# Kernel optimization log

Hardware: AMD Instinct MI355X
Metric: run time of the kernel (lower is better)

## Reference

```python
import jax, jax.numpy as jnp
import numpy as np

B, NDOC, L, E = 32, 4, 512, 512
SCALE = np.float32(1.0 / np.sqrt(E))
NEG_INF = np.float32(-1e9)


def setup_inputs() -> dict:
    key = jax.random.key(0)
    k1, k2, k3, k4, k5, k6 = jax.random.split(key, 6)
    return {
        "x1": jax.random.normal(k1, (B, L, E), dtype=jnp.float32),
        "x2": jax.random.normal(k2, (B, NDOC, L, E), dtype=jnp.float32),
        "x1_len": jax.random.randint(k3, (B,), 0, L, dtype=jnp.int64),
        "x2_len": jax.random.randint(k4, (B, NDOC), 0, L, dtype=jnp.int64),
        "fusion_w": jax.random.normal(k5, (2 * E, E), dtype=jnp.float32) * 0.02,
        "fusion_b": jnp.zeros((E,), dtype=jnp.float32),
        "out_w": jax.random.normal(k6, (8 * E, 2 * E), dtype=jnp.float32) * 0.02,
        "out_b": jnp.zeros((2 * E,), dtype=jnp.float32),
    }


def reference(x1, x2, x1_len, x2_len, fusion_w, fusion_b, out_w, out_b):
    # Faithful to torch .repeat(1,4,...): concatenate 4 full copies along batch,
    # so attention row i pairs x1[i % B] with x2[i // 4, i % 4].
    x1_rep = jnp.tile(x1, (NDOC, 1, 1))          # [4B, L, E]
    x2_r = x2.reshape(-1, L, E)                  # [4B, L, E]

    x1_len_r = jnp.tile(x1_len, NDOC)            # [4B] (same tiling as x1_rep)
    x2_len_r = x2_len.reshape(-1)                # [4B]
    pos = jnp.arange(L)
    q_mask = pos[None, :] < x1_len_r[:, None]    # [4B, L]
    k_mask = pos[None, :] < x2_len_r[:, None]    # [4B, L]
    mask = q_mask[:, :, None] & k_mask[:, None, :]  # [4B, L, L]

    # scaled-dot-product attention with masked_fill(mask==0, -1e9)
    scores = jnp.einsum('bqe,bke->bqk', x1_rep, x2_r) * SCALE  # [4B, L, L]
    scores = jnp.where(mask, scores, NEG_INF)
    attn = jax.nn.softmax(scores, axis=-1)
    x1_att = jnp.einsum('bqk,bke->bqe', attn, x2_r)            # [4B, L, E]

    cat = jnp.concatenate([x1_rep - x1_att, x1_rep * x1_att], axis=-1)  # [4B, L, 2E]
    fus = jax.nn.relu(cat @ fusion_w + fusion_b)                        # [4B, L, E]

    x1_mean = jnp.mean(fus, axis=1)              # [4B, E]
    x1_max = jnp.max(fus, axis=1)                # [4B, E]
    pooled = jnp.concatenate([x1_mean.reshape(B, -1), x1_max.reshape(B, -1)], axis=-1)  # [B, 8E]
    out = jax.nn.relu(pooled @ out_w + out_b)    # [B, 2E]
    return out, attn
```

## Files before the change

### kernel.cpp

```cpp
#include <hip/hip_runtime.h>
#include <cstddef>

#define BATCH 32
#define NB    128
#define LL    512
#define EE    512
#define SCALE 0.044194173824159216f
#define NEG_INF -1e9f

typedef __attribute__((ext_vector_type(4))) float f32x4;
typedef __attribute__((ext_vector_type(8))) short s16x8;
typedef __attribute__((ext_vector_type(4))) unsigned short u16x4;

__device__ __forceinline__ unsigned short f2b(float f) {
    unsigned u = __float_as_uint(f);
    u += 0x7FFFu + ((u >> 16) & 1u);
    return (unsigned short)(u >> 16);
}
__device__ __forceinline__ float b2f(unsigned short h) {
    return __uint_as_float(((unsigned)h) << 16);
}

__device__ __forceinline__ void gld_lds16(const unsigned short* g, unsigned short* l) {
    __builtin_amdgcn_global_load_lds(
        (const __attribute__((address_space(1))) void*)g,
        (__attribute__((address_space(3))) void*)l, 16, 0, 0);
}

__global__ __launch_bounds__(256) void k_cvt_x1(
    const float* __restrict__ x1, unsigned short* __restrict__ x1bf)
{
    const size_t idx = (size_t)blockIdx.x * 256 + threadIdx.x;
    f32x4 v = *(const f32x4*)(x1 + idx * 4);
    u16x4 o = { f2b(v[0]), f2b(v[1]), f2b(v[2]), f2b(v[3]) };
    *(u16x4*)(x1bf + idx * 4) = o;
}

__global__ __launch_bounds__(256) void k_cvt_x2(
    const float* __restrict__ x2,
    unsigned short* __restrict__ x2bf, unsigned short* __restrict__ x2t)
{
    __shared__ float T[64][65];
    const int i = blockIdx.z, kb = blockIdx.y * 64, eb = blockIdx.x * 64;
    const float* src = x2 + (size_t)i * LL * EE;
    unsigned short* db = x2bf + (size_t)i * LL * EE;
    unsigned short* dt = x2t  + (size_t)i * LL * EE;
    const int t = threadIdx.x, r16 = t >> 4, c4 = (t & 15) * 4;
#pragma unroll
    for (int p = 0; p < 4; ++p) {
        int row = p * 16 + r16;
        f32x4 v = *(const f32x4*)(src + (size_t)(kb + row) * EE + eb + c4);
        T[row][c4] = v[0]; T[row][c4+1] = v[1]; T[row][c4+2] = v[2]; T[row][c4+3] = v[3];
        u16x4 o = { f2b(v[0]), f2b(v[1]), f2b(v[2]), f2b(v[3]) };
        *(u16x4*)(db + (size_t)(kb + row) * EE + eb + c4) = o;
    }
    __syncthreads();
#pragma unroll
    for (int p = 0; p < 4; ++p) {
        int erow = p * 16 + r16;
        u16x4 o = { f2b(T[c4][erow]), f2b(T[c4+1][erow]),
                    f2b(T[c4+2][erow]), f2b(T[c4+3][erow]) };
        *(u16x4*)(dt + (size_t)(eb + erow) * LL + kb + c4) = o;
    }
}

__global__ __launch_bounds__(256) void k_cvt_fw(
    const float* __restrict__ fw, unsigned short* __restrict__ fwt)
{
    __shared__ float T[64][65];
    const int jb = blockIdx.y * 64, eb = blockIdx.x * 64;
    const int t = threadIdx.x, r16 = t >> 4, c4 = (t & 15) * 4;
#pragma unroll
    for (int p = 0; p < 4; ++p) {
        int row = p * 16 + r16;
        f32x4 v = *(const f32x4*)(fw + (size_t)(jb + row) * EE + eb + c4);
        T[row][c4] = v[0]; T[row][c4+1] = v[1]; T[row][c4+2] = v[2]; T[row][c4+3] = v[3];
    }
    __syncthreads();
#pragma unroll
    for (int p = 0; p < 4; ++p) {
        int erow = p * 16 + r16;
#pragma unroll
        for (int k = 0; k < 4; ++k) {
            int jold = jb + c4 + k;
            int jn = (jold < 512) ? (2 * jold) : (2 * (jold - 512) + 1);
            fwt[(size_t)(eb + erow) * 1024 + jn] = f2b(T[c4 + k][erow]);
        }
    }
}

__global__ __launch_bounds__(256) void k_scores_mfma(
    const unsigned short* __restrict__ x1bf,
    const unsigned short* __restrict__ x2bf,
    const int* __restrict__ x1_len, const int* __restrict__ x2_len,
    float* __restrict__ attn)
{
    __shared__ unsigned short Al[128 * 32];
    __shared__ unsigned short Bl[128 * 32];
    const int i  = blockIdx.x;
    const int q0 = (blockIdx.y >> 2) * 128;
    const int k0 = (blockIdx.y & 3) * 128;
    const unsigned short* Ag = x1bf + (size_t)(i & 31) * LL * EE;
    const unsigned short* Bg = x2bf + (size_t)i * LL * EE;
    const int t = threadIdx.x, lane = t & 63;
    const int w = t >> 6, wrow = w >> 1, wcol = w & 1;
    const int m = lane & 15, quad = lane >> 4;
    const int lrow = lane >> 2, lcol = (lane & 3) * 8;

    f32x4 acc[4][4];
#pragma unroll
    for (int r = 0; r < 4; ++r)
#pragma unroll
        for (int c = 0; c < 4; ++c) acc[r][c] = (f32x4){0.f, 0.f, 0.f, 0.f};

    for (int e0 = 0; e0 < EE; e0 += 32) {
#pragma unroll
        for (int c = 0; c < 2; ++c) {
            const int s = c * 4 + w;
            gld_lds16(Ag + (size_t)(q0 + s * 16 + lrow) * EE + e0 + lcol, &Al[s * 512]);
            gld_lds16(Bg + (size_t)(k0 + s * 16 + lrow) * EE + e0 + lcol, &Bl[s * 512]);
        }
        __syncthreads();
        s16x8 af[4], bfr[4];
#pragma unroll
        for (int rt = 0; rt < 4; ++rt)
            af[rt] = *(const s16x8*)&Al[(wrow * 64 + rt * 16 + m) * 32 + quad * 8];
#pragma unroll
        for (int ct = 0; ct < 4; ++ct)
            bfr[ct] = *(const s16x8*)&Bl[(wcol * 64 + ct * 16 + m) * 32 + quad * 8];
#pragma unroll
        for (int rt = 0; rt < 4; ++rt)
#pragma unroll
            for (int ct = 0; ct < 4; ++ct)
                acc[rt][ct] = __builtin_amdgcn_mfma_f32_16x16x32_bf16(
                    af[rt], bfr[ct], acc[rt][ct], 0, 0, 0);
        __syncthreads();
    }

    const int qlen = x1_len[i & 31];
    const int klen = x2_len[i];
    float* op = attn + (size_t)i * LL * LL;
#pragma unroll
    for (int rt = 0; rt < 4; ++rt) {
#pragma unroll
        for (int reg = 0; reg < 4; ++reg) {
            const int q = q0 + wrow * 64 + rt * 16 + quad * 4 + reg;
            const bool qok = q < qlen;
#pragma unroll
            for (int ct = 0; ct < 4; ++ct) {
                const int k = k0 + wcol * 64 + ct * 16 + m;
                float v = (qok && k < klen) ? acc[rt][ct][reg] * SCALE : NEG_INF;
                op[(size_t)q * LL + k] = v;
            }
        }
    }
}

__global__ __launch_bounds__(256) void k_softmax(
    float* __restrict__ attn, unsigned short* __restrict__ attnbf)
{
    const int row  = blockIdx.x * 4 + (threadIdx.x >> 6);
    const int lane = threadIdx.x & 63;
    float* p = attn + (size_t)row * LL + lane * 8;
    float4 v0 = *(float4*)p;
    float4 v1 = *(float4*)(p + 4);
    float mx = fmaxf(fmaxf(fmaxf(v0.x, v0.y), fmaxf(v0.z, v0.w)),
                     fmaxf(fmaxf(v1.x, v1.y), fmaxf(v1.z, v1.w)));
#pragma unroll
    for (int o = 32; o > 0; o >>= 1) mx = fmaxf(mx, __shfl_xor(mx, o));
    v0.x = __expf(v0.x - mx); v0.y = __expf(v0.y - mx);
    v0.z = __expf(v0.z - mx); v0.w = __expf(v0.w - mx);
    v1.x = __expf(v1.x - mx); v1.y = __expf(v1.y - mx);
    v1.z = __expf(v1.z - mx); v1.w = __expf(v1.w - mx);
    float s = v0.x + v0.y + v0.z + v0.w + v1.x + v1.y + v1.z + v1.w;
#pragma unroll
    for (int o = 32; o > 0; o >>= 1) s += __shfl_xor(s, o);
    const float inv = 1.0f / s;
    v0.x *= inv; v0.y *= inv; v0.z *= inv; v0.w *= inv;
    v1.x *= inv; v1.y *= inv; v1.z *= inv; v1.w *= inv;
    *(float4*)p = v0;
    *(float4*)(p + 4) = v1;
    unsigned short* pb = attnbf + (size_t)row * LL + lane * 8;
    u16x4 o0 = { f2b(v0.x), f2b(v0.y), f2b(v0.z), f2b(v0.w) };
    u16x4 o1 = { f2b(v1.x), f2b(v1.y), f2b(v1.z), f2b(v1.w) };
    *(u16x4*)pb       = o0;
    *(u16x4*)(pb + 4) = o1;
}

__global__ __launch_bounds__(256) void k_pv_mfma(
    const unsigned short* __restrict__ attnbf,
    const unsigned short* __restrict__ x2t,
    const unsigned short* __restrict__ x1bf,
    unsigned short* __restrict__ Cbuf)
{
    __shared__ unsigned short Al[128 * 32];
    __shared__ unsigned short Bl[128 * 32];
    const int i  = blockIdx.x;
    const int q0 = (blockIdx.y >> 2) * 128;
    const int e0 = (blockIdx.y & 3) * 128;
    const unsigned short* Ag = attnbf + (size_t)i * LL * LL;
    const unsigned short* Bg = x2t   + (size_t)i * LL * EE;
    const int t = threadIdx.x, lane = t & 63;
    const int w = t >> 6, wrow = w >> 1, wcol = w & 1;
    const int m = lane & 15, quad = lane >> 4;
    const int lrow = lane >> 2, lcol = (lane & 3) * 8;

    f32x4 acc[4][4];
#pragma unroll
    for (int r = 0; r < 4; ++r)
#pragma unroll
        for (int c = 0; c < 4; ++c) acc[r][c] = (f32x4){0.f, 0.f, 0.f, 0.f};

    for (int kk0 = 0; kk0 < LL; kk0 += 32) {
#pragma unroll
        for (int c = 0; c < 2; ++c) {
            const int s = c * 4 + w;
            gld_lds16(Ag + (size_t)(q0 + s * 16 + lrow) * LL + kk0 + lcol, &Al[s * 512]);
            gld_lds16(Bg + (size_t)(e0 + s * 16 + lrow) * LL + kk0 + lcol, &Bl[s * 512]);
        }
        __syncthreads();
        s16x8 af[4], bfr[4];
#pragma unroll
        for (int rt = 0; rt < 4; ++rt)
            af[rt] = *(const s16x8*)&Al[(wrow * 64 + rt * 16 + m) * 32 + quad * 8];
#pragma unroll
        for (int ct = 0; ct < 4; ++ct)
            bfr[ct] = *(const s16x8*)&Bl[(wcol * 64 + ct * 16 + m) * 32 + quad * 8];
#pragma unroll
        for (int rt = 0; rt < 4; ++rt)
#pragma unroll
            for (int ct = 0; ct < 4; ++ct)
                acc[rt][ct] = __builtin_amdgcn_mfma_f32_16x16x32_bf16(
                    af[rt], bfr[ct], acc[rt][ct], 0, 0, 0);
        __syncthreads();
    }

    const unsigned short* x1p = x1bf + (size_t)(i & 31) * LL * EE;
    unsigned short* Cb = Cbuf + (size_t)i * LL * 1024;
#pragma unroll
    for (int rt = 0; rt < 4; ++rt) {
#pragma unroll
        for (int reg = 0; reg < 4; ++reg) {
            const int l = q0 + wrow * 64 + rt * 16 + quad * 4 + reg;
#pragma unroll
            for (int ct = 0; ct < 4; ++ct) {
                const int e = e0 + wcol * 64 + ct * 16 + m;
                float att = acc[rt][ct][reg];
                float xv  = b2f(x1p[(size_t)l * EE + e]);
                unsigned pr = (unsigned)f2b(xv - att) | ((unsigned)f2b(xv * att) << 16);
                *(unsigned*)(Cb + (size_t)l * 1024 + 2 * e) = pr;
            }
        }
    }
}

__global__ __launch_bounds__(256) void k_fuse_mfma(
    const unsigned short* __restrict__ Cbuf,
    const unsigned short* __restrict__ fwt,
    const float* __restrict__ fb,
    float* __restrict__ pmean, float* __restrict__ pmax)
{
    __shared__ unsigned short Al[128 * 32];
    __shared__ unsigned short Bl[128 * 32];
    __shared__ float psum[2][128];
    __shared__ float pmx[2][128];
    const int i  = blockIdx.x;
    const int lt = blockIdx.y >> 2;
    const int e0 = (blockIdx.y & 3) * 128;
    const unsigned short* Ab = Cbuf + ((size_t)i * LL + lt * 128) * 1024;
    const int t = threadIdx.x, lane = t & 63;
    const int w = t >> 6, wrow = w >> 1, wcol = w & 1;
    const int m = lane & 15, quad = lane >> 4;
    const int lrow = lane >> 2, lcol = (lane & 3) * 8;

    float bias[4];
#pragma unroll
    for (int ct = 0; ct < 4; ++ct) bias[ct] = fb[e0 + wcol * 64 + ct * 16 + m];
    float csum[4] = {0.f, 0.f, 0.f, 0.f};
    float cmax[4] = {-3e38f, -3e38f, -3e38f, -3e38f};

    f32x4 acc[4][4];
#pragma unroll
    for (int r = 0; r < 4; ++r)
#pragma unroll
        for (int c = 0; c < 4; ++c) acc[r][c] = (f32x4){0.f, 0.f, 0.f, 0.f};

    for (int j0 = 0; j0 < 1024; j0 += 32) {
#pragma unroll
        for (int c = 0; c < 2; ++c) {
            const int s = c * 4 + w;
            gld_lds16(Ab + (size_t)(s * 16 + lrow) * 1024 + j0 + lcol, &Al[s * 512]);
            gld_lds16(fwt + (size_t)(e0 + s * 16 + lrow) * 1024 + j0 + lcol, &Bl[s * 512]);
        }
        __syncthreads();
        s16x8 af[4], bfr[4];
#pragma unroll
        for (int rt = 0; rt < 4; ++rt)
            af[rt] = *(const s16x8*)&Al[(wrow * 64 + rt * 16 + m) * 32 + quad * 8];
#pragma unroll
        for (int ct = 0; ct < 4; ++ct)
            bfr[ct] = *(const s16x8*)&Bl[(wcol * 64 + ct * 16 + m) * 32 + quad * 8];
#pragma unroll
        for (int rt = 0; rt < 4; ++rt)
#pragma unroll
            for (int ct = 0; ct < 4; ++ct)
                acc[rt][ct] = __builtin_amdgcn_mfma_f32_16x16x32_bf16(
                    af[rt], bfr[ct], acc[rt][ct], 0, 0, 0);
        __syncthreads();
    }
#pragma unroll
    for (int rt = 0; rt < 4; ++rt)
#pragma unroll
        for (int reg = 0; reg < 4; ++reg)
#pragma unroll
            for (int ct = 0; ct < 4; ++ct) {
                float f = fmaxf(acc[rt][ct][reg] + bias[ct], 0.f);
                csum[ct] += f;
                cmax[ct] = fmaxf(cmax[ct], f);
            }
#pragma unroll
    for (int ct = 0; ct < 4; ++ct) {
        csum[ct] += __shfl_xor(csum[ct], 16);
        csum[ct] += __shfl_xor(csum[ct], 32);
        cmax[ct] = fmaxf(cmax[ct], __shfl_xor(cmax[ct], 16));
        cmax[ct] = fmaxf(cmax[ct], __shfl_xor(cmax[ct], 32));
    }
    if (quad == 0) {
#pragma unroll
        for (int ct = 0; ct < 4; ++ct) {
            psum[wrow][wcol * 64 + ct * 16 + m] = csum[ct];
            pmx[wrow][wcol * 64 + ct * 16 + m] = cmax[ct];
        }
    }
    __syncthreads();
    if (t < 128) {
        float s  = psum[0][t] + psum[1][t];
        float mx = fmaxf(pmx[0][t], pmx[1][t]);
        pmean[((size_t)i * 4 + lt) * EE + e0 + t] = s;
        pmax[((size_t)i * 4 + lt) * EE + e0 + t]  = mx;
    }
}

__global__ __launch_bounds__(256) void k_out_split(
    const float* __restrict__ pmean, const float* __restrict__ pmax,
    const float* __restrict__ ow, float* __restrict__ partial)
{
    __shared__ float ps[256];
    const int kc = blockIdx.x;
    const int b  = blockIdx.y;
    const int t  = threadIdx.x;
    const int j  = kc * 256 + t;
    const int jj = (j < 2048) ? j : j - 2048;
    const int ii = 4 * b + (jj >> 9);
    const int e  = jj & 511;
    float v;
    if (j < 2048) {
        const float* bp = pmean + (size_t)ii * 4 * EE + e;
        v = (bp[0] + bp[512] + bp[1024] + bp[1536]) * (1.0f / 512.0f);
    } else {
        const float* bp = pmax + (size_t)ii * 4 * EE + e;
        v = fmaxf(fmaxf(bp[0], bp[512]), fmaxf(bp[1024], bp[1536]));
    }
    ps[t] = v;
    __syncthreads();
    f32x4 acc = {0.f, 0.f, 0.f, 0.f};
    const float* wp = ow + (size_t)kc * 256 * 1024 + t * 4;
#pragma unroll 8
    for (int q = 0; q < 256; ++q) {
        f32x4 w4 = *(const f32x4*)(wp + (size_t)q * 1024);
        float p = ps[q];
        acc[0] = fmaf(p, w4[0], acc[0]);
        acc[1] = fmaf(p, w4[1], acc[1]);
        acc[2] = fmaf(p, w4[2], acc[2]);
        acc[3] = fmaf(p, w4[3], acc[3]);
    }
    *(f32x4*)(partial + ((size_t)kc * 32 + b) * 1024 + t * 4) = acc;
}

__global__ __launch_bounds__(256) void k_out_final(
    const float* __restrict__ partial, const float* __restrict__ ob,
    float* __restrict__ out)
{
    const int idx = blockIdx.x * 256 + threadIdx.x;
    const int b = idx >> 10, o = idx & 1023;
    float s = ob[o];
#pragma unroll
    for (int kc = 0; kc < 16; ++kc)
        s += partial[((size_t)kc * 32 + b) * 1024 + o];
    out[idx] = fmaxf(s, 0.f);
}

extern "C" void kernel_launch(void* const* d_in, const int* in_sizes, int n_in,
                              void* d_out, int out_size, void* d_ws, size_t ws_size,
                              hipStream_t stream)
{
    const float* x1     = (const float*)d_in[0];
    const float* x2     = (const float*)d_in[1];
    const int*   x1_len = (const int*)d_in[2];
    const int*   x2_len = (const int*)d_in[3];
    const float* fw     = (const float*)d_in[4];
    const float* fb     = (const float*)d_in[5];
    const float* ow     = (const float*)d_in[6];
    const float* ob     = (const float*)d_in[7];

    float* out  = (float*)d_out;
    float* attn = out + (size_t)BATCH * 1024;

    char* wp = (char*)d_ws;
    unsigned short* x1bf   = (unsigned short*)wp; wp += (size_t)BATCH * LL * EE * 2;
    unsigned short* x2bf   = (unsigned short*)wp; wp += (size_t)NB * LL * EE * 2;
    unsigned short* x2t    = (unsigned short*)wp; wp += (size_t)NB * LL * EE * 2;
    unsigned short* attnbf = (unsigned short*)wp; wp += (size_t)NB * LL * LL * 2;
    unsigned short* Cbuf   = (unsigned short*)wp; wp += (size_t)NB * LL * 1024 * 2;
    unsigned short* fwt    = (unsigned short*)wp; wp += (size_t)EE * 1024 * 2;
    float* pmean   = (float*)wp; wp += (size_t)NB * 4 * EE * 4;
    float* pmax    = (float*)wp; wp += (size_t)NB * 4 * EE * 4;
    float* partial = (float*)wp; wp += (size_t)16 * BATCH * 1024 * 4;

    k_cvt_x1<<<dim3(BATCH * LL * EE / 4 / 256), 256, 0, stream>>>(x1, x1bf);
    k_cvt_x2<<<dim3(8, 8, NB), 256, 0, stream>>>(x2, x2bf, x2t);
    k_cvt_fw<<<dim3(8, 16), 256, 0, stream>>>(fw, fwt);
    k_scores_mfma<<<dim3(128, 16), 256, 0, stream>>>(x1bf, x2bf, x1_len, x2_len, attn);
    k_softmax<<<dim3(NB * LL / 4), 256, 0, stream>>>(attn, attnbf);
    k_pv_mfma<<<dim3(128, 16), 256, 0, stream>>>(attnbf, x2t, x1bf, Cbuf);
    k_fuse_mfma<<<dim3(128, 16), 256, 0, stream>>>(Cbuf, fwt, fb, pmean, pmax);
    k_out_split<<<dim3(16, BATCH), 256, 0, stream>>>(pmean, pmax, ow, partial);
    k_out_final<<<dim3(BATCH * 1024 / 256), 256, 0, stream>>>(partial, ob, out);
}
```

Baseline: 637.0 us.

## Fuse scores, softmax and PV into one full-row attention kernel

```diff
diff --git a/kernel.cpp b/kernel.cpp
--- a/kernel.cpp
+++ b/kernel.cpp
@@ -89,23 +89,30 @@
     }
 }
 
-__global__ __launch_bounds__(256) void k_scores_mfma(
+__global__ __launch_bounds__(1024, 4) void k_attn(
     const unsigned short* __restrict__ x1bf,
     const unsigned short* __restrict__ x2bf,
+    const unsigned short* __restrict__ x2t,
     const int* __restrict__ x1_len, const int* __restrict__ x2_len,
-    float* __restrict__ attn)
-{
-    __shared__ unsigned short Al[128 * 32];
-    __shared__ unsigned short Bl[128 * 32];
+    float* __restrict__ attn, unsigned short* __restrict__ Cbuf)
+{
+    __shared__ __align__(16) char smem[147456];
+    unsigned short* Ast = (unsigned short*)smem;
+    unsigned short* Bst = (unsigned short*)(smem + 8192);
+    unsigned short* Bpv = (unsigned short*)(smem + 131072);
+    float* rowred = (float*)(smem + 131072);
+    float* rowst  = (float*)(smem + 131072 + 4096);
+
     const int i  = blockIdx.x;
-    const int q0 = (blockIdx.y >> 2) * 128;
-    const int k0 = (blockIdx.y & 3) * 128;
+    const int q0 = blockIdx.y * 128;
     const unsigned short* Ag = x1bf + (size_t)(i & 31) * LL * EE;
     const unsigned short* Bg = x2bf + (size_t)i * LL * EE;
+    const unsigned short* Vg = x2t  + (size_t)i * LL * EE;
     const int t = threadIdx.x, lane = t & 63;
-    const int w = t >> 6, wrow = w >> 1, wcol = w & 1;
+    const int w = t >> 6;
     const int m = lane & 15, quad = lane >> 4;
     const int lrow = lane >> 2, lcol = (lane & 3) * 8;
+    const int wrow = w >> 3, wcol = w & 7;
 
     f32x4 acc[4][4];
 #pragma unroll
@@ -114,20 +121,18 @@
         for (int c = 0; c < 4; ++c) acc[r][c] = (f32x4){0.f, 0.f, 0.f, 0.f};
 
     for (int e0 = 0; e0 < EE; e0 += 32) {
-#pragma unroll
-        for (int c = 0; c < 2; ++c) {
-            const int s = c * 4 + w;
-            gld_lds16(Ag + (size_t)(q0 + s * 16 + lrow) * EE + e0 + lcol, &Al[s * 512]);
-            gld_lds16(Bg + (size_t)(k0 + s * 16 + lrow) * EE + e0 + lcol, &Bl[s * 512]);
-        }
+        if (w < 8)
+            gld_lds16(Ag + (size_t)(q0 + w * 16 + lrow) * EE + e0 + lcol, &Ast[w * 512]);
+        gld_lds16(Bg + (size_t)((2 * w) * 16 + lrow) * EE + e0 + lcol, &Bst[(2 * w) * 512]);
+        gld_lds16(Bg + (size_t)((2 * w + 1) * 16 + lrow) * EE + e0 + lcol, &Bst[(2 * w + 1) * 512]);
         __syncthreads();
         s16x8 af[4], bfr[4];
 #pragma unroll
         for (int rt = 0; rt < 4; ++rt)
-            af[rt] = *(const s16x8*)&Al[(wrow * 64 + rt * 16 + m) * 32 + quad * 8];
+            af[rt] = *(const s16x8*)&Ast[(wrow * 64 + rt * 16 + m) * 32 + quad * 8];
 #pragma unroll
         for (int ct = 0; ct < 4; ++ct)
-            bfr[ct] = *(const s16x8*)&Bl[(wcol * 64 + ct * 16 + m) * 32 + quad * 8];
+            bfr[ct] = *(const s16x8*)&Bst[(wcol * 64 + ct * 16 + m) * 32 + quad * 8];
 #pragma unroll
         for (int rt = 0; rt < 4; ++rt)
 #pragma unroll
@@ -139,118 +144,135 @@
 
     const int qlen = x1_len[i & 31];
     const int klen = x2_len[i];
-    float* op = attn + (size_t)i * LL * LL;
-#pragma unroll
-    for (int rt = 0; rt < 4; ++rt) {
-#pragma unroll
-        for (int reg = 0; reg < 4; ++reg) {
-            const int q = q0 + wrow * 64 + rt * 16 + quad * 4 + reg;
-            const bool qok = q < qlen;
-#pragma unroll
-            for (int ct = 0; ct < 4; ++ct) {
-                const int k = k0 + wcol * 64 + ct * 16 + m;
-                float v = (qok && k < klen) ? acc[rt][ct][reg] * SCALE : NEG_INF;
-                op[(size_t)q * LL + k] = v;
-            }
-        }
-    }
-}
-
-__global__ __launch_bounds__(256) void k_softmax(
-    float* __restrict__ attn, unsigned short* __restrict__ attnbf)
-{
-    const int row  = blockIdx.x * 4 + (threadIdx.x >> 6);
-    const int lane = threadIdx.x & 63;
-    float* p = attn + (size_t)row * LL + lane * 8;
-    float4 v0 = *(float4*)p;
-    float4 v1 = *(float4*)(p + 4);
-    float mx = fmaxf(fmaxf(fmaxf(v0.x, v0.y), fmaxf(v0.z, v0.w)),
-                     fmaxf(fmaxf(v1.x, v1.y), fmaxf(v1.z, v1.w)));
-#pragma unroll
-    for (int o = 32; o > 0; o >>= 1) mx = fmaxf(mx, __shfl_xor(mx, o));
-    v0.x = __expf(v0.x - mx); v0.y = __expf(v0.y - mx);
-    v0.z = __expf(v0.z - mx); v0.w = __expf(v0.w - mx);
-    v1.x = __expf(v1.x - mx); v1.y = __expf(v1.y - mx);
-    v1.z = __expf(v1.z - mx); v1.w = __expf(v1.w - mx);
-    float s = v0.x + v0.y + v0.z + v0.w + v1.x + v1.y + v1.z + v1.w;
-#pragma unroll
-    for (int o = 32; o > 0; o >>= 1) s += __shfl_xor(s, o);
-    const float inv = 1.0f / s;
-    v0.x *= inv; v0.y *= inv; v0.z *= inv; v0.w *= inv;
-    v1.x *= inv; v1.y *= inv; v1.z *= inv; v1.w *= inv;
-    *(float4*)p = v0;
-    *(float4*)(p + 4) = v1;
-    unsigned short* pb = attnbf + (size_t)row * LL + lane * 8;
-    u16x4 o0 = { f2b(v0.x), f2b(v0.y), f2b(v0.z), f2b(v0.w) };
-    u16x4 o1 = { f2b(v1.x), f2b(v1.y), f2b(v1.z), f2b(v1.w) };
-    *(u16x4*)pb       = o0;
-    *(u16x4*)(pb + 4) = o1;
-}
-
-__global__ __launch_bounds__(256) void k_pv_mfma(
-    const unsigned short* __restrict__ attnbf,
-    const unsigned short* __restrict__ x2t,
-    const unsigned short* __restrict__ x1bf,
-    unsigned short* __restrict__ Cbuf)
-{
-    __shared__ unsigned short Al[128 * 32];
-    __shared__ unsigned short Bl[128 * 32];
-    const int i  = blockIdx.x;
-    const int q0 = (blockIdx.y >> 2) * 128;
-    const int e0 = (blockIdx.y & 3) * 128;
-    const unsigned short* Ag = attnbf + (size_t)i * LL * LL;
-    const unsigned short* Bg = x2t   + (size_t)i * LL * EE;
-    const int t = threadIdx.x, lane = t & 63;
-    const int w = t >> 6, wrow = w >> 1, wcol = w & 1;
-    const int m = lane & 15, quad = lane >> 4;
-    const int lrow = lane >> 2, lcol = (lane & 3) * 8;
-
-    f32x4 acc[4][4];
-#pragma unroll
-    for (int r = 0; r < 4; ++r)
-#pragma unroll
-        for (int c = 0; c < 4; ++c) acc[r][c] = (f32x4){0.f, 0.f, 0.f, 0.f};
-
-    for (int kk0 = 0; kk0 < LL; kk0 += 32) {
-#pragma unroll
-        for (int c = 0; c < 2; ++c) {
-            const int s = c * 4 + w;
-            gld_lds16(Ag + (size_t)(q0 + s * 16 + lrow) * LL + kk0 + lcol, &Al[s * 512]);
-            gld_lds16(Bg + (size_t)(e0 + s * 16 + lrow) * LL + kk0 + lcol, &Bl[s * 512]);
-        }
-        __syncthreads();
-        s16x8 af[4], bfr[4];
-#pragma unroll
-        for (int rt = 0; rt < 4; ++rt)
-            af[rt] = *(const s16x8*)&Al[(wrow * 64 + rt * 16 + m) * 32 + quad * 8];
-#pragma unroll
-        for (int ct = 0; ct < 4; ++ct)
-            bfr[ct] = *(const s16x8*)&Bl[(wcol * 64 + ct * 16 + m) * 32 + quad * 8];
-#pragma unroll
-        for (int rt = 0; rt < 4; ++rt)
-#pragma unroll
-            for (int ct = 0; ct < 4; ++ct)
-                acc[rt][ct] = __builtin_amdgcn_mfma_f32_16x16x32_bf16(
-                    af[rt], bfr[ct], acc[rt][ct], 0, 0, 0);
-        __syncthreads();
-    }
-
-    const unsigned short* x1p = x1bf + (size_t)(i & 31) * LL * EE;
-    unsigned short* Cb = Cbuf + (size_t)i * LL * 1024;
-#pragma unroll
-    for (int rt = 0; rt < 4; ++rt) {
+
+#pragma unroll
+    for (int rt = 0; rt < 4; ++rt)
 #pragma unroll
         for (int reg = 0; reg < 4; ++reg) {
             const int l = q0 + wrow * 64 + rt * 16 + quad * 4 + reg;
+            const bool qok = l < qlen;
 #pragma unroll
             for (int ct = 0; ct < 4; ++ct) {
-                const int e = e0 + wcol * 64 + ct * 16 + m;
-                float att = acc[rt][ct][reg];
-                float xv  = b2f(x1p[(size_t)l * EE + e]);
-                unsigned pr = (unsigned)f2b(xv - att) | ((unsigned)f2b(xv * att) << 16);
-                *(unsigned*)(Cb + (size_t)l * 1024 + 2 * e) = pr;
-            }
-        }
+                const int k = wcol * 64 + ct * 16 + m;
+                acc[rt][ct][reg] = (qok && k < klen) ? acc[rt][ct][reg] * SCALE : NEG_INF;
+            }
+        }
+
+#pragma unroll
+    for (int rt = 0; rt < 4; ++rt)
+#pragma unroll
+        for (int reg = 0; reg < 4; ++reg) {
+            float v = fmaxf(fmaxf(acc[rt][0][reg], acc[rt][1][reg]),
+                            fmaxf(acc[rt][2][reg], acc[rt][3][reg]));
+            v = fmaxf(v, __shfl_xor(v, 1));
+            v = fmaxf(v, __shfl_xor(v, 2));
+            v = fmaxf(v, __shfl_xor(v, 4));
+            v = fmaxf(v, __shfl_xor(v, 8));
+            if (m == 0)
+                rowred[wcol * 128 + wrow * 64 + rt * 16 + quad * 4 + reg] = v;
+        }
+    __syncthreads();
+    if (t < 128) {
+        float mx = rowred[t];
+#pragma unroll
+        for (int c = 1; c < 8; ++c) mx = fmaxf(mx, rowred[c * 128 + t]);
+        rowst[t] = mx;
+    }
+    __syncthreads();
+
+#pragma unroll
+    for (int rt = 0; rt < 4; ++rt)
+#pragma unroll
+        for (int reg = 0; reg < 4; ++reg) {
+            const int lloc = wrow * 64 + rt * 16 + quad * 4 + reg;
+            const float mx = rowst[lloc];
+            float s = 0.f;
+#pragma unroll
+            for (int ct = 0; ct < 4; ++ct) {
+                float p = __expf(acc[rt][ct][reg] - mx);
+                acc[rt][ct][reg] = p;
+                s += p;
+            }
+            s += __shfl_xor(s, 1);
+            s += __shfl_xor(s, 2);
+            s += __shfl_xor(s, 4);
+            s += __shfl_xor(s, 8);
+            if (m == 0) rowred[wcol * 128 + lloc] = s;
+        }
+    __syncthreads();
+    if (t < 128) {
+        float s = 0.f;
+#pragma unroll
+        for (int c = 0; c < 8; ++c) s += rowred[c * 128 + t];
+        rowst[t] = 1.0f / s;
+    }
+    __syncthreads();
+
+    float* op = attn + (size_t)i * LL * LL;
+#pragma unroll
+    for (int rt = 0; rt < 4; ++rt)
+#pragma unroll
+        for (int reg = 0; reg < 4; ++reg) {
+            const int lloc = wrow * 64 + rt * 16 + quad * 4 + reg;
+            const float inv = rowst[lloc];
+#pragma unroll
+            for (int ct = 0; ct < 4; ++ct) {
+                const int k = wcol * 64 + ct * 16 + m;
+                float p = acc[rt][ct][reg] * inv;
+                op[(size_t)(q0 + lloc) * LL + k] = p;
+                unsigned off = (unsigned)(lloc * 1024 + k * 2) ^ (unsigned)((lloc & 7) << 4);
+                *(unsigned short*)(smem + off) = f2b(p);
+            }
+        }
+    __syncthreads();
+
+    const int pwr = w >> 2, pwc = w & 3;
+    unsigned short* Cb = Cbuf + (size_t)i * LL * 1024;
+#pragma unroll
+    for (int eh = 0; eh < 2; ++eh) {
+        f32x4 acc2[2][4];
+#pragma unroll
+        for (int r = 0; r < 2; ++r)
+#pragma unroll
+            for (int c = 0; c < 4; ++c) acc2[r][c] = (f32x4){0.f, 0.f, 0.f, 0.f};
+
+        for (int k0 = 0; k0 < LL; k0 += 32) {
+            gld_lds16(Vg + (size_t)(eh * 256 + w * 16 + lrow) * LL + k0 + lcol, &Bpv[w * 512]);
+            __syncthreads();
+            s16x8 paf[2], pbf[4];
+#pragma unroll
+            for (int rt = 0; rt < 2; ++rt) {
+                const int lr = pwr * 32 + rt * 16 + m;
+                unsigned off = (unsigned)(lr * 1024 + (k0 + quad * 8) * 2)
+                               ^ (unsigned)((lr & 7) << 4);
+                paf[rt] = *(const s16x8*)(smem + off);
+            }
+#pragma unroll
+            for (int ct = 0; ct < 4; ++ct)
+                pbf[ct] = *(const s16x8*)&Bpv[(pwc * 64 + ct * 16 + m) * 32 + quad * 8];
+#pragma unroll
+            for (int rt = 0; rt < 2; ++rt)
+#pragma unroll
+                for (int ct = 0; ct < 4; ++ct)
+                    acc2[rt][ct] = __builtin_amdgcn_mfma_f32_16x16x32_bf16(
+                        paf[rt], pbf[ct], acc2[rt][ct], 0, 0, 0);
+            __syncthreads();
+        }
+
+#pragma unroll
+        for (int rt = 0; rt < 2; ++rt)
+#pragma unroll
+            for (int reg = 0; reg < 4; ++reg) {
+                const int l = q0 + pwr * 32 + rt * 16 + quad * 4 + reg;
+#pragma unroll
+                for (int ct = 0; ct < 4; ++ct) {
+                    const int e = eh * 256 + pwc * 64 + ct * 16 + m;
+                    float att = acc2[rt][ct][reg];
+                    float xv  = b2f(Ag[(size_t)l * EE + e]);
+                    unsigned pr = (unsigned)f2b(xv - att) | ((unsigned)f2b(xv * att) << 16);
+                    *(unsigned*)(Cb + (size_t)l * 1024 + 2 * e) = pr;
+                }
+            }
     }
 }
 
@@ -410,7 +432,6 @@
     unsigned short* x1bf   = (unsigned short*)wp; wp += (size_t)BATCH * LL * EE * 2;
     unsigned short* x2bf   = (unsigned short*)wp; wp += (size_t)NB * LL * EE * 2;
     unsigned short* x2t    = (unsigned short*)wp; wp += (size_t)NB * LL * EE * 2;
-    unsigned short* attnbf = (unsigned short*)wp; wp += (size_t)NB * LL * LL * 2;
     unsigned short* Cbuf   = (unsigned short*)wp; wp += (size_t)NB * LL * 1024 * 2;
     unsigned short* fwt    = (unsigned short*)wp; wp += (size_t)EE * 1024 * 2;
     float* pmean   = (float*)wp; wp += (size_t)NB * 4 * EE * 4;
@@ -420,9 +441,7 @@
     k_cvt_x1<<<dim3(BATCH * LL * EE / 4 / 256), 256, 0, stream>>>(x1, x1bf);
     k_cvt_x2<<<dim3(8, 8, NB), 256, 0, stream>>>(x2, x2bf, x2t);
     k_cvt_fw<<<dim3(8, 16), 256, 0, stream>>>(fw, fwt);
-    k_scores_mfma<<<dim3(128, 16), 256, 0, stream>>>(x1bf, x2bf, x1_len, x2_len, attn);
-    k_softmax<<<dim3(NB * LL / 4), 256, 0, stream>>>(attn, attnbf);
-    k_pv_mfma<<<dim3(128, 16), 256, 0, stream>>>(attnbf, x2t, x1bf, Cbuf);
+    k_attn<<<dim3(128, 4), 1024, 0, stream>>>(x1bf, x2bf, x2t, x1_len, x2_len, attn, Cbuf);
     k_fuse_mfma<<<dim3(128, 16), 256, 0, stream>>>(Cbuf, fwt, fb, pmean, pmax);
     k_out_split<<<dim3(16, BATCH), 256, 0, stream>>>(pmean, pmax, ow, partial);
     k_out_final<<<dim3(BATCH * 1024 / 256), 256, 0, stream>>>(partial, ob, out);
```

Result: faster. 578.5 us (-9.2%).
